# Kernel optimization log

Hardware: AMD Instinct MI355X
Metric: run time of the kernel (lower is better)

## Reference

```python
import jax, jax.numpy as jnp
import numpy as np

B, S, D, H = 4, 2048, 1024, 16
DK = D // H


def setup_inputs() -> dict:
    key = jax.random.key(0)
    ks = jax.random.split(key, 11)
    s = 1.0 / np.sqrt(D)
    return {
        "Q": jax.random.normal(ks[0], (B, S, D), jnp.float32),
        "K": jax.random.normal(ks[1], (B, S, D), jnp.float32),
        "V": jax.random.normal(ks[2], (B, S, D), jnp.float32),
        "Wq": jax.random.normal(ks[3], (D, D), jnp.float32) * s,
        "bq": jnp.zeros((D,), jnp.float32),
        "Wk": jax.random.normal(ks[4], (D, D), jnp.float32) * s,
        "bk": jnp.zeros((D,), jnp.float32),
        "Wv": jax.random.normal(ks[5], (D, D), jnp.float32) * s,
        "bv": jnp.zeros((D,), jnp.float32),
        "Wo": jax.random.normal(ks[6], (D, D), jnp.float32) * s,
        "bo": jnp.zeros((D,), jnp.float32),
    }


def reference(Q, K, V, Wq, bq, Wk, bk, Wv, bv, Wo, bo):
    # projections: [B,S,D] -> [B,H,S,DK]
    def split_heads(x):
        return x.reshape(B, -1, H, DK).transpose(0, 2, 1, 3)

    q = split_heads(Q @ Wq.T + bq)
    k = split_heads(K @ Wk.T + bk)
    v = split_heads(V @ Wv.T + bv)
    scale = 1.0 / jnp.sqrt(jnp.float32(DK))
    scores = jnp.einsum("bhqd,bhkd->bhqk", q, k) * scale
    attn = jax.nn.softmax(scores, axis=-1)  # dropout = identity (eval)
    out = jnp.einsum("bhqk,bhkd->bhqd", attn, v)
    out = out.transpose(0, 2, 1, 3).reshape(B, -1, D)
    return out @ Wo.T + bo
```

## Files before the change

### kernel.cpp

```cpp
#include <hip/hip_runtime.h>

#define SEQ    2048
#define DMODEL 1024
#define NH     16
#define DKH    64
#define MROWS  8192

typedef unsigned short u16;
typedef __bf16    bf16x8 __attribute__((ext_vector_type(8)));
typedef _Float16  f16x4  __attribute__((ext_vector_type(4)));
typedef _Float16  f16x8  __attribute__((ext_vector_type(8)));
typedef __fp16    hf16x2 __attribute__((ext_vector_type(2)));
typedef float     f32x4  __attribute__((ext_vector_type(4)));
typedef u16       u16x4  __attribute__((ext_vector_type(4)));
typedef u16       u16x8  __attribute__((ext_vector_type(8)));

__device__ __forceinline__ u16 f2b(float f) {
  union { float f; unsigned u; } v; v.f = f;
  unsigned r = v.u + 0x7fffu + ((v.u >> 16) & 1u);
  return (u16)(r >> 16);
}
__device__ __forceinline__ unsigned pk_f16(float a, float b) {
  union { hf16x2 h; unsigned u; } v;
  v.h = __builtin_amdgcn_cvt_pkrtz(a, b);
  return v.u;
}

__global__ __launch_bounds__(256) void cvt3_kernel(
    const float* __restrict__ a0, const float* __restrict__ a1, const float* __restrict__ a2,
    u16* o0, u16* o1, u16* o2, int n4) {
  int i = blockIdx.x * 256 + threadIdx.x;
  if (i >= n4) return;
  const float* in; u16* out;
  switch (blockIdx.y) {
    case 0: in = a0; out = o0; break;
    case 1: in = a1; out = o1; break;
    default: in = a2; out = o2; break;
  }
  f32x4 v = ((const f32x4*)in)[i];
  u16x4 o;
  o.x = f2b(v.x); o.y = f2b(v.y); o.z = f2b(v.z); o.w = f2b(v.w);
  ((u16x4*)out)[i] = o;
}
__global__ __launch_bounds__(256) void cvt4_kernel(
    const float* __restrict__ a0, const float* __restrict__ a1,
    const float* __restrict__ a2, const float* __restrict__ a3,
    u16* o0, u16* o1, u16* o2, u16* o3, int n4) {
  int i = blockIdx.x * 256 + threadIdx.x;
  if (i >= n4) return;
  const float* in; u16* out;
  switch (blockIdx.y) {
    case 0: in = a0; out = o0; break;
    case 1: in = a1; out = o1; break;
    case 2: in = a2; out = o2; break;
    default: in = a3; out = o3; break;
  }
  f32x4 v = ((const f32x4*)in)[i];
  u16x4 o;
  o.x = f2b(v.x); o.y = f2b(v.y); o.z = f2b(v.z); o.w = f2b(v.w);
  ((u16x4*)out)[i] = o;
}

__device__ __forceinline__ void gemm_body(
    const u16* __restrict__ A, const u16* __restrict__ W,
    const float* __restrict__ bias, void* __restrict__ outp, int mode, float oscale,
    int bx, int by, u16* smem) {
  u16* As = smem;
  u16* Bs = smem + 8192;

  const int tid  = threadIdx.x;
  const int w    = tid >> 6;
  const int lane = tid & 63;
  const int l15  = lane & 15;
  const int quad = lane >> 4;
  const int x7   = l15 & 7;
  const int n0 = bx * 128;
  const int m0 = by * 128;
  const int wm = (w >> 1) * 64;
  const int wn = (w & 1) * 64;

  f32x4 acc[4][4];
#pragma unroll
  for (int mt = 0; mt < 4; ++mt)
#pragma unroll
    for (int nt = 0; nt < 4; ++nt)
      acc[mt][nt] = (f32x4){0.f, 0.f, 0.f, 0.f};

  const int srow = w * 32 + (lane >> 3);
  const int scol = (((lane & 7) ^ (lane >> 3)) * 8);
  const size_t arow = (size_t)(m0 + srow) * DMODEL;
  const size_t brow = (size_t)(n0 + srow) * DMODEL;

  for (int ks = 0; ks < DMODEL / 64; ++ks) {
    const int k0 = ks * 64;
#pragma unroll
    for (int i = 0; i < 4; ++i) {
      __builtin_amdgcn_global_load_lds(
          (const __attribute__((address_space(1))) void*)(A + arow + (size_t)i * 8 * DMODEL + k0 + scol),
          (__attribute__((address_space(3))) void*)(&As[(w * 4 + i) * 512]),
          16, 0, 0);
      __builtin_amdgcn_global_load_lds(
          (const __attribute__((address_space(1))) void*)(W + brow + (size_t)i * 8 * DMODEL + k0 + scol),
          (__attribute__((address_space(3))) void*)(&Bs[(w * 4 + i) * 512]),
          16, 0, 0);
    }
    __syncthreads();
#pragma unroll
    for (int kk = 0; kk < 64; kk += 32) {
      const int kc = kk >> 3;
      bf16x8 af[4], bfr[4];
#pragma unroll
      for (int mt = 0; mt < 4; ++mt) {
        const int row = wm + mt * 16 + l15;
        af[mt] = *(const bf16x8*)&As[row * 64 + (((kc + quad) ^ (row & 7)) * 8)];
      }
#pragma unroll
      for (int nt = 0; nt < 4; ++nt) {
        const int row = wn + nt * 16 + l15;
        bfr[nt] = *(const bf16x8*)&Bs[row * 64 + (((kc + quad) ^ (row & 7)) * 8)];
      }
#pragma unroll
      for (int mt = 0; mt < 4; ++mt)
#pragma unroll
        for (int nt = 0; nt < 4; ++nt)
          acc[mt][nt] = __builtin_amdgcn_mfma_f32_16x16x32_bf16(af[mt], bfr[nt], acc[mt][nt], 0, 0, 0);
    }
    __syncthreads();
  }

  if (mode == 3) {
    float* o = (float*)outp;
#pragma unroll
    for (int nt = 0; nt < 4; ++nt) {
      const int col = n0 + wn + nt * 16 + l15;
      const float bv = bias[col];
#pragma unroll
      for (int mt = 0; mt < 4; ++mt) {
        const int mbase = m0 + wm + mt * 16 + quad * 4;
        f32x4 c = acc[mt][nt];
#pragma unroll
        for (int r = 0; r < 4; ++r)
          o[(size_t)(mbase + r) * DMODEL + col] = (c[r] + bv) * oscale;
      }
    }
    return;
  }

  u16* Cs = smem;
  if (mode == 0) {
#pragma unroll
    for (int nt = 0; nt < 4; ++nt) {
      const int col = n0 + wn + nt * 16 + l15;
      const float bv = bias[col];
      const int nl = wn + nt * 16 + l15;
      const int n8 = nl >> 3;
#pragma unroll
      for (int mt = 0; mt < 4; ++mt) {
        const int mb = wm + mt * 16 + quad * 4;
        f32x4 c = acc[mt][nt];
#pragma unroll
        for (int r = 0; r < 4; ++r) {
          const int m = mb + r;
          Cs[m * 128 + ((n8 ^ (m & 7)) * 8) + x7] = f2b((c[r] + bv) * oscale);
        }
      }
    }
  } else {
#pragma unroll
    for (int nt = 0; nt < 4; ++nt) {
      const int col = n0 + wn + nt * 16 + l15;
      const float bv = bias[col];
      const int nl = wn + nt * 16 + l15;
#pragma unroll
      for (int mt = 0; mt < 4; ++mt) {
        const int mb = wm + mt * 16 + quad * 4;
        f32x4 c = acc[mt][nt];
        union { u16x4 u4; unsigned u2[2]; } pk;
        pk.u2[0] = pk_f16((c[0] + bv) * oscale, (c[1] + bv) * oscale);
        pk.u2[1] = pk_f16((c[2] + bv) * oscale, (c[3] + bv) * oscale);
        *(u16x4*)&Cs[nl * 128 + (((mb >> 3) ^ (nl & 7)) * 8) + (mb & 7)] = pk.u4;
      }
    }
  }
  __syncthreads();

  const int rl   = tid >> 1;
  const int half = tid & 1;
  const int b    = m0 >> 11;
  if (mode == 0) {
    u16* o = (u16*)outp;
    const int s = (m0 + rl) & 2047;
    const int h = (n0 >> 6) + half;
    u16* orow = o + (((size_t)(b * NH + h) * SEQ + s)) * DKH;
#pragma unroll
    for (int j = 0; j < 8; ++j) {
      u16x8 v = *(const u16x8*)&Cs[rl * 128 + (((half * 8 + j) ^ (rl & 7)) * 8)];
      *(u16x8*)&orow[j * 8] = v;
    }
  } else {
    u16* o = (u16*)outp;
    const int plane = b * 1024 + n0 + rl;
    const int scol2 = (m0 & 2047) + half * 64;
    u16* orow = o + (size_t)plane * SEQ + scol2;
#pragma unroll
    for (int j = 0; j < 8; ++j) {
      u16x8 v = *(const u16x8*)&Cs[rl * 128 + (((half * 8 + j) ^ (rl & 7)) * 8)];
      *(u16x8*)&orow[j * 8] = v;
    }
  }
}

__device__ __forceinline__ void xcd_remap(int& bx, int& by) {
  const int lin = (int)blockIdx.x + (int)blockIdx.y * 8;
  const int xcd = lin & 7;
  const int idx = lin >> 3;
  by = xcd * 8 + (idx >> 3);
  bx = idx & 7;
}

__global__ __launch_bounds__(256) void gemm_kernel(
    const u16* __restrict__ A, const u16* __restrict__ W,
    const float* __restrict__ bias, void* __restrict__ outp, int mode, float oscale) {
  __shared__ __align__(16) u16 smem[16384];
  int bx, by; xcd_remap(bx, by);
  gemm_body(A, W, bias, outp, mode, oscale, bx, by, smem);
}

__global__ __launch_bounds__(256) void qkv_gemm_kernel(
    const u16* Aq, const u16* Ak, const u16* Av,
    const u16* Wq, const u16* Wk, const u16* Wv,
    const float* bq, const float* bk, const float* bv,
    u16* oq, u16* ok, u16* ov, float qscale) {
  __shared__ __align__(16) u16 smem[16384];
  const u16* A; const u16* W; const float* bias; u16* o; int mode; float sc;
  switch (blockIdx.z) {
    case 0:  A = Aq; W = Wq; bias = bq; o = oq; mode = 0; sc = qscale; break;
    case 1:  A = Ak; W = Wk; bias = bk; o = ok; mode = 0; sc = 1.f;    break;
    default: A = Av; W = Wv; bias = bv; o = ov; mode = 2; sc = 1.f;    break;
  }
  int bx, by; xcd_remap(bx, by);
  gemm_body(A, W, bias, o, mode, sc, bx, by, smem);
}

__global__ __launch_bounds__(128, 2) void attn_kernel(
    const u16* __restrict__ qh, const u16* __restrict__ kh,
    const u16* __restrict__ vt, u16* __restrict__ ao) {
  __shared__ __align__(16) u16 smem[8192];
  u16* Ks = smem;
  u16* Vs = smem + 4096;

  const int tid  = threadIdx.x;
  const int w    = tid >> 6;
  const int lane = tid & 63;
  const int l15  = lane & 15;
  const int quad = lane >> 4;
  const int x7   = l15 & 7;
  const int bh = blockIdx.y;
  const int q0 = blockIdx.x * 128;

  const u16* kbase = kh + (size_t)bh * SEQ * DKH;
  const u16* vbase = vt + (size_t)bh * DKH * SEQ;

  const int lr  = lane >> 3;
  const int lc8 = ((lane & 7) ^ lr) * 8;

  const int rbase = l15 * 64;
  const int c0 = (quad ^ x7) * 8;
  const int c1 = c0 ^ 32;

  bf16x8 qf[4][2];
#pragma unroll
  for (int g = 0; g < 4; ++g) {
    const u16* qrow = qh + ((size_t)bh * SEQ + q0 + w * 64 + g * 16 + l15) * DKH;
    qf[g][0] = *(const bf16x8*)(qrow + quad * 8);
    qf[g][1] = *(const bf16x8*)(qrow + 32 + quad * 8);
  }

  f32x4 o[4][4];
#pragma unroll
  for (int g = 0; g < 4; ++g)
#pragma unroll
    for (int dt = 0; dt < 4; ++dt) o[g][dt] = (f32x4){0.f, 0.f, 0.f, 0.f};
  float lsum[4] = {0.f, 0.f, 0.f, 0.f};

  for (int kt = 0; kt < SEQ / 64; ++kt) {
    const int k0 = kt * 64;
#pragma unroll
    for (int i = 0; i < 4; ++i) {
      const int rowb = i * 16 + w * 8;
      const int krow = rowb + lr;
      const int kkey = ((krow >> 4) & 1) * 32 + ((krow >> 2) & 3) * 8 +
                       (krow >> 5) * 4 + (krow & 3);
      __builtin_amdgcn_global_load_lds(
          (const __attribute__((address_space(1))) void*)(kbase + (size_t)(k0 + kkey) * DKH + lc8),
          (__attribute__((address_space(3))) void*)(&Ks[rowb * 64]), 16, 0, 0);
      __builtin_amdgcn_global_load_lds(
          (const __attribute__((address_space(1))) void*)(vbase + (size_t)(rowb + lr) * SEQ + k0 + lc8),
          (__attribute__((address_space(3))) void*)(&Vs[rowb * 64]), 16, 0, 0);
    }
    __syncthreads();

    bf16x8 kf[4][2];
#pragma unroll
    for (int nt = 0; nt < 4; ++nt) {
      kf[nt][0] = *(const bf16x8*)&Ks[nt * 1024 + rbase + c0];
      kf[nt][1] = *(const bf16x8*)&Ks[nt * 1024 + rbase + c1];
    }

    f16x8 pb[4][2];
#pragma unroll
    for (int g = 0; g < 4; ++g) {
      f32x4 sf[4];
      __builtin_amdgcn_s_setprio(1);
#pragma unroll
      for (int nt = 0; nt < 4; ++nt) {
        f32x4 a = (f32x4){-8.f, -8.f, -8.f, -8.f};
        a = __builtin_amdgcn_mfma_f32_16x16x32_bf16(kf[nt][0], qf[g][0], a, 0, 0, 0);
        a = __builtin_amdgcn_mfma_f32_16x16x32_bf16(kf[nt][1], qf[g][1], a, 0, 0, 0);
        sf[nt] = a;
      }
      __builtin_amdgcn_s_setprio(0);
      unsigned d0[4], d1[4];
#pragma unroll
      for (int nt = 0; nt < 4; ++nt) {
        float p0 = __builtin_amdgcn_exp2f(sf[nt][0]);
        float p1 = __builtin_amdgcn_exp2f(sf[nt][1]);
        float p2 = __builtin_amdgcn_exp2f(sf[nt][2]);
        float p3 = __builtin_amdgcn_exp2f(sf[nt][3]);
        lsum[g] += (p0 + p1) + (p2 + p3);
        d0[nt] = pk_f16(p0, p1);
        d1[nt] = pk_f16(p2, p3);
      }
#pragma unroll
      for (int b2 = 0; b2 < 2; ++b2) {
        union { f16x8 h; unsigned u[4]; } u;
        u.u[0] = d0[b2]; u.u[1] = d1[b2]; u.u[2] = d0[b2 + 2]; u.u[3] = d1[b2 + 2];
        pb[g][b2] = u.h;
      }
    }

    __builtin_amdgcn_s_setprio(1);
#pragma unroll
    for (int dt = 0; dt < 4; ++dt) {
#pragma unroll
      for (int b2 = 0; b2 < 2; ++b2) {
        const int vaddr = (dt * 16 + l15) * 64 + (((b2 * 4 + quad) ^ x7) * 8);
        f16x8 vf = *(const f16x8*)&Vs[vaddr];
#pragma unroll
        for (int g = 0; g < 4; ++g)
          o[g][dt] = __builtin_amdgcn_mfma_f32_16x16x32_f16(vf, pb[g][b2], o[g][dt], 0, 0, 0);
      }
    }
    __builtin_amdgcn_s_setprio(0);
    __syncthreads();
  }

  float inv[4];
#pragma unroll
  for (int g = 0; g < 4; ++g) {
    float l = lsum[g];
    l += __shfl_xor(l, 16);
    l += __shfl_xor(l, 32);
    inv[g] = 1.0f / l;
  }

#pragma unroll
  for (int g = 0; g < 4; ++g) {
    const int q = w * 64 + g * 16 + l15;
#pragma unroll
    for (int dt = 0; dt < 4; ++dt) {
      const int dk = dt * 16 + quad * 4;
      u16x4 pk;
      pk.x = f2b(o[g][dt][0] * inv[g]);
      pk.y = f2b(o[g][dt][1] * inv[g]);
      pk.z = f2b(o[g][dt][2] * inv[g]);
      pk.w = f2b(o[g][dt][3] * inv[g]);
      *(u16x4*)&smem[q * 64 + (((dk >> 3) ^ (q & 7)) * 8) + (dk & 7)] = pk;
    }
  }
  __syncthreads();

  const int b = bh >> 4;
  const int h = bh & 15;
  const int rr = tid >> 3;
  const int cc = tid & 7;
#pragma unroll
  for (int j = 0; j < 8; ++j) {
    const int row = j * 16 + rr;
    u16x8 v = *(const u16x8*)&smem[row * 64 + ((cc ^ (row & 7)) * 8)];
    u16* orow = ao + ((size_t)(b * SEQ + q0 + row)) * DMODEL + h * DKH + cc * 8;
    *(u16x8*)orow = v;
  }
}

extern "C" void kernel_launch(void* const* d_in, const int* in_sizes, int n_in,
                              void* d_out, int out_size, void* d_ws, size_t ws_size,
                              hipStream_t stream) {
  const float* Q  = (const float*)d_in[0];
  const float* K  = (const float*)d_in[1];
  const float* V  = (const float*)d_in[2];
  const float* Wq = (const float*)d_in[3];
  const float* bq = (const float*)d_in[4];
  const float* Wk = (const float*)d_in[5];
  const float* bk = (const float*)d_in[6];
  const float* Wv = (const float*)d_in[7];
  const float* bv = (const float*)d_in[8];
  const float* Wo = (const float*)d_in[9];
  const float* bo = (const float*)d_in[10];

  const float QSCALE = 0.18033688011112042f;
  char* ws = (char*)d_ws;
  const size_t MB = 1ull << 20;
  const int nA4 = (MROWS * DMODEL) / 4;
  const int nW4 = (DMODEL * DMODEL) / 4;
  dim3 gg(DMODEL / 128, MROWS / 128);
  dim3 ag(SEQ / 128, 4 * NH);

  if (ws_size >= 104 * MB) {
    u16* Xq  = (u16*)(ws);
    u16* Xk  = (u16*)(ws + 16 * MB);
    u16* Xv  = (u16*)(ws + 32 * MB);
    u16* Wqb = (u16*)(ws + 48 * MB);
    u16* Wkb = (u16*)(ws + 50 * MB);
    u16* Wvb = (u16*)(ws + 52 * MB);
    u16* Wob = (u16*)(ws + 54 * MB);
    u16* qh  = (u16*)(ws + 56 * MB);
    u16* kh  = (u16*)(ws + 72 * MB);
    u16* vth = (u16*)(ws + 88 * MB);
    u16* AO  = Xq;

    cvt4_kernel<<<dim3(nW4 / 256, 4), 256, 0, stream>>>(Wq, Wk, Wv, Wo, Wqb, Wkb, Wvb, Wob, nW4);
    cvt3_kernel<<<dim3(nA4 / 256, 3), 256, 0, stream>>>(Q, K, V, Xq, Xk, Xv, nA4);
    qkv_gemm_kernel<<<dim3(8, 64, 3), 256, 0, stream>>>(
        Xq, Xk, Xv, Wqb, Wkb, Wvb, bq, bk, bv, qh, kh, vth, QSCALE);
    attn_kernel<<<ag, 128, 0, stream>>>(qh, kh, vth, AO);
    gemm_kernel<<<gg, 256, 0, stream>>>(AO, Wob, bo, d_out, 3, 1.0f);
  } else {
    u16* X   = (u16*)(ws);
    u16* Wqb = (u16*)(ws + 16 * MB);
    u16* Wkb = (u16*)(ws + 18 * MB);
    u16* Wvb = (u16*)(ws + 20 * MB);
    u16* Wob = (u16*)(ws + 22 * MB);
    u16* qh  = (u16*)(ws + 24 * MB);
    u16* kh  = (u16*)(ws + 40 * MB);
    u16* vth = (u16*)(ws + 56 * MB);

    cvt4_kernel<<<dim3(nW4 / 256, 4), 256, 0, stream>>>(Wq, Wk, Wv, Wo, Wqb, Wkb, Wvb, Wob, nW4);
    cvt3_kernel<<<dim3(nA4 / 256, 1), 256, 0, stream>>>(Q, Q, Q, X, X, X, nA4);
    gemm_kernel<<<gg, 256, 0, stream>>>(X, Wqb, bq, qh, 0, QSCALE);
    cvt3_kernel<<<dim3(nA4 / 256, 1), 256, 0, stream>>>(K, K, K, X, X, X, nA4);
    gemm_kernel<<<gg, 256, 0, stream>>>(X, Wkb, bk, kh, 0, 1.0f);
    cvt3_kernel<<<dim3(nA4 / 256, 1), 256, 0, stream>>>(V, V, V, X, X, X, nA4);
    gemm_kernel<<<gg, 256, 0, stream>>>(X, Wvb, bv, vth, 2, 1.0f);
    attn_kernel<<<ag, 128, 0, stream>>>(qh, kh, vth, X);
    gemm_kernel<<<gg, 256, 0, stream>>>(X, Wob, bo, d_out, 3, 1.0f);
  }
}
```

Measured before the change: 342.6 us.

## Split attention KV range across wave pairs with LDS reduction and remap blocks

Doubles the attention block to 256 threads (4 waves). Two waves handle the 128 query rows over the first half of the key sequence and two handle the second half, so each block runs 16 KV iterations instead of 32. The partial O accumulators and row sums are merged through LDS. Block indices are also remapped so that neighbouring blocks spread across (b,h) heads, which targets XCD/L2 locality. The aim is more waves in flight per block, at the cost of extra LDS, an extra reduction step with syncs, and possible lower occupancy from the larger shared memory footprint.

```diff
diff --git a/kernel.cpp b/kernel.cpp
--- a/kernel.cpp
+++ b/kernel.cpp
@@ -242,12 +242,10 @@
   gemm_body(A, W, bias, o, mode, sc, bx, by, smem);
 }
 
-__global__ __launch_bounds__(128, 2) void attn_kernel(
+__global__ __launch_bounds__(256, 4) void attn_kernel(
     const u16* __restrict__ qh, const u16* __restrict__ kh,
     const u16* __restrict__ vt, u16* __restrict__ ao) {
-  __shared__ __align__(16) u16 smem[8192];
-  u16* Ks = smem;
-  u16* Vs = smem + 4096;
+  __shared__ __align__(16) u16 smem[16896];
 
   const int tid  = threadIdx.x;
   const int w    = tid >> 6;
@@ -255,8 +253,10 @@
   const int l15  = lane & 15;
   const int quad = lane >> 4;
   const int x7   = l15 & 7;
-  const int bh = blockIdx.y;
-  const int q0 = blockIdx.x * 128;
+
+  const int lin = (int)blockIdx.x + ((int)blockIdx.y << 4);
+  const int bh  = (lin & 7) * 8 + ((lin >> 3) >> 4);
+  const int q0  = ((lin >> 3) & 15) * 128;
 
   const u16* kbase = kh + (size_t)bh * SEQ * DKH;
   const u16* vbase = vt + (size_t)bh * DKH * SEQ;
@@ -268,10 +268,13 @@
   const int c0 = (quad ^ x7) * 8;
   const int c1 = c0 ^ 32;
 
+  const int qhalf = w & 1;
+  const int khalf = w >> 1;
+
   bf16x8 qf[4][2];
 #pragma unroll
   for (int g = 0; g < 4; ++g) {
-    const u16* qrow = qh + ((size_t)bh * SEQ + q0 + w * 64 + g * 16 + l15) * DKH;
+    const u16* qrow = qh + ((size_t)bh * SEQ + q0 + qhalf * 64 + g * 16 + l15) * DKH;
     qf[g][0] = *(const bf16x8*)(qrow + quad * 8);
     qf[g][1] = *(const bf16x8*)(qrow + 32 + quad * 8);
   }
@@ -283,22 +286,36 @@
     for (int dt = 0; dt < 4; ++dt) o[g][dt] = (f32x4){0.f, 0.f, 0.f, 0.f};
   float lsum[4] = {0.f, 0.f, 0.f, 0.f};
 
-  for (int kt = 0; kt < SEQ / 64; ++kt) {
-    const int k0 = kt * 64;
-#pragma unroll
-    for (int i = 0; i < 4; ++i) {
-      const int rowb = i * 16 + w * 8;
-      const int krow = rowb + lr;
-      const int kkey = ((krow >> 4) & 1) * 32 + ((krow >> 2) & 3) * 8 +
-                       (krow >> 5) * 4 + (krow & 3);
-      __builtin_amdgcn_global_load_lds(
-          (const __attribute__((address_space(1))) void*)(kbase + (size_t)(k0 + kkey) * DKH + lc8),
-          (__attribute__((address_space(3))) void*)(&Ks[rowb * 64]), 16, 0, 0);
-      __builtin_amdgcn_global_load_lds(
-          (const __attribute__((address_space(1))) void*)(vbase + (size_t)(rowb + lr) * SEQ + k0 + lc8),
-          (__attribute__((address_space(3))) void*)(&Vs[rowb * 64]), 16, 0, 0);
+  const int sth = w & 1;
+  const int stv = w >> 1;
+  u16* dstb = smem + sth * 8192 + stv * 4096;
+
+  for (int kt = 0; kt < SEQ / 128; ++kt) {
+    const int sk0 = sth * 1024 + kt * 64;
+    if (stv == 0) {
+#pragma unroll
+      for (int i = 0; i < 8; ++i) {
+        const int rowb = i * 8;
+        const int krow = rowb + lr;
+        const int kkey = ((krow >> 4) & 1) * 32 + ((krow >> 2) & 3) * 8 +
+                         (krow >> 5) * 4 + (krow & 3);
+        __builtin_amdgcn_global_load_lds(
+            (const __attribute__((address_space(1))) void*)(kbase + (size_t)(sk0 + kkey) * DKH + lc8),
+            (__attribute__((address_space(3))) void*)(&dstb[rowb * 64]), 16, 0, 0);
+      }
+    } else {
+#pragma unroll
+      for (int i = 0; i < 8; ++i) {
+        const int rowb = i * 8;
+        __builtin_amdgcn_global_load_lds(
+            (const __attribute__((address_space(1))) void*)(vbase + (size_t)(rowb + lr) * SEQ + sk0 + lc8),
+            (__attribute__((address_space(3))) void*)(&dstb[rowb * 64]), 16, 0, 0);
+      }
     }
     __syncthreads();
+
+    const u16* Ks = smem + khalf * 8192;
+    const u16* Vs = Ks + 4096;
 
     bf16x8 kf[4][2];
 #pragma unroll
@@ -355,38 +372,76 @@
     __syncthreads();
   }
 
-  float inv[4];
+  float lh[4];
 #pragma unroll
   for (int g = 0; g < 4; ++g) {
     float l = lsum[g];
     l += __shfl_xor(l, 16);
     l += __shfl_xor(l, 32);
-    inv[g] = 1.0f / l;
-  }
-
-#pragma unroll
-  for (int g = 0; g < 4; ++g) {
-    const int q = w * 64 + g * 16 + l15;
-#pragma unroll
-    for (int dt = 0; dt < 4; ++dt) {
-      const int dk = dt * 16 + quad * 4;
-      u16x4 pk;
-      pk.x = f2b(o[g][dt][0] * inv[g]);
-      pk.y = f2b(o[g][dt][1] * inv[g]);
-      pk.z = f2b(o[g][dt][2] * inv[g]);
-      pk.w = f2b(o[g][dt][3] * inv[g]);
-      *(u16x4*)&smem[q * 64 + (((dk >> 3) ^ (q & 7)) * 8) + (dk & 7)] = pk;
+    lh[g] = l;
+  }
+
+  float* ldsO = (float*)smem;
+  float* ldsL = (float*)&smem[16384];
+  const int p = qhalf;
+  if (w >= 2) {
+#pragma unroll
+    for (int g = 0; g < 4; ++g) {
+#pragma unroll
+      for (int dt = 0; dt < 4; ++dt) {
+        const int q  = g * 16 + l15;
+        const int dk = dt * 16 + quad * 4;
+        *(f32x4*)&ldsO[p * 4096 + q * 64 + (dk ^ ((q & 7) << 3))] = o[g][dt];
+      }
+    }
+    if (quad == 0) {
+#pragma unroll
+      for (int g = 0; g < 4; ++g) ldsL[p * 64 + g * 16 + l15] = lh[g];
     }
   }
   __syncthreads();
 
-  const int b = bh >> 4;
-  const int h = bh & 15;
+  float inv[4];
+  if (w < 2) {
+#pragma unroll
+    for (int g = 0; g < 4; ++g) {
+#pragma unroll
+      for (int dt = 0; dt < 4; ++dt) {
+        const int q  = g * 16 + l15;
+        const int dk = dt * 16 + quad * 4;
+        f32x4 t = *(const f32x4*)&ldsO[p * 4096 + q * 64 + (dk ^ ((q & 7) << 3))];
+        o[g][dt] += t;
+      }
+      inv[g] = 1.0f / (lh[g] + ldsL[p * 64 + g * 16 + l15]);
+    }
+  }
+  __syncthreads();
+
+  if (w < 2) {
+#pragma unroll
+    for (int g = 0; g < 4; ++g) {
+      const int q = qhalf * 64 + g * 16 + l15;
+#pragma unroll
+      for (int dt = 0; dt < 4; ++dt) {
+        const int dk = dt * 16 + quad * 4;
+        u16x4 pk;
+        pk.x = f2b(o[g][dt][0] * inv[g]);
+        pk.y = f2b(o[g][dt][1] * inv[g]);
+        pk.z = f2b(o[g][dt][2] * inv[g]);
+        pk.w = f2b(o[g][dt][3] * inv[g]);
+        *(u16x4*)&smem[q * 64 + (((dk >> 3) ^ (q & 7)) * 8) + (dk & 7)] = pk;
+      }
+    }
+  }
+  __syncthreads();
+
+  const int b  = bh >> 4;
+  const int h  = bh & 15;
   const int rr = tid >> 3;
   const int cc = tid & 7;
 #pragma unroll
-  for (int j = 0; j < 8; ++j) {
-    const int row = j * 16 + rr;
+  for (int j = 0; j < 4; ++j) {
+    const int row = j * 32 + rr;
     u16x8 v = *(const u16x8*)&smem[row * 64 + ((cc ^ (row & 7)) * 8)];
     u16* orow = ao + ((size_t)(b * SEQ + q0 + row)) * DMODEL + h * DKH + cc * 8;
     *(u16x8*)orow = v;
@@ -433,7 +488,7 @@
     cvt3_kernel<<<dim3(nA4 / 256, 3), 256, 0, stream>>>(Q, K, V, Xq, Xk, Xv, nA4);
     qkv_gemm_kernel<<<dim3(8, 64, 3), 256, 0, stream>>>(
         Xq, Xk, Xv, Wqb, Wkb, Wvb, bq, bk, bv, qh, kh, vth, QSCALE);
-    attn_kernel<<<ag, 128, 0, stream>>>(qh, kh, vth, AO);
+    attn_kernel<<<ag, 256, 0, stream>>>(qh, kh, vth, AO);
     gemm_kernel<<<gg, 256, 0, stream>>>(AO, Wob, bo, d_out, 3, 1.0f);
   } else {
     u16* X   = (u16*)(ws);
@@ -452,7 +507,7 @@
     gemm_kernel<<<gg, 256, 0, stream>>>(X, Wkb, bk, kh, 0, 1.0f);
     cvt3_kernel<<<dim3(nA4 / 256, 1), 256, 0, stream>>>(V, V, V, X, X, X, nA4);
     gemm_kernel<<<gg, 256, 0, stream>>>(X, Wvb, bv, vth, 2, 1.0f);
-    attn_kernel<<<ag, 128, 0, stream>>>(qh, kh, vth, X);
+    attn_kernel<<<ag, 256, 0, stream>>>(qh, kh, vth, X);
     gemm_kernel<<<gg, 256, 0, stream>>>(X, Wob, bo, d_out, 3, 1.0f);
   }
 }
```

Measured after the change: 650.9 us. +90.0%, slower.

## Double-buffer K/V tiles in attention kernel with async global-to-LDS prefetch

Applied to the files above, without the earlier changes.

The attention kernel gets a second LDS buffer. It issues the global_load_lds copies for the next K/V tile before computing the current one, and uses vmcnt waits plus raw barriers instead of __syncthreads. This is meant to hide global memory latency behind the MFMA work. LDS use per block doubles to 32KB, which may limit occupancy. Correctness also relies on the manual vmcnt(8) counting matching the eight loads each stage issues.

```diff
diff --git a/kernel.cpp b/kernel.cpp
--- a/kernel.cpp
+++ b/kernel.cpp
@@ -245,9 +245,7 @@
 __global__ __launch_bounds__(128, 2) void attn_kernel(
     const u16* __restrict__ qh, const u16* __restrict__ kh,
     const u16* __restrict__ vt, u16* __restrict__ ao) {
-  __shared__ __align__(16) u16 smem[8192];
-  u16* Ks = smem;
-  u16* Vs = smem + 4096;
+  __shared__ __align__(16) u16 smem[16384];
 
   const int tid  = threadIdx.x;
   const int w    = tid >> 6;
@@ -275,16 +273,16 @@
     qf[g][0] = *(const bf16x8*)(qrow + quad * 8);
     qf[g][1] = *(const bf16x8*)(qrow + 32 + quad * 8);
   }
-
-  f32x4 o[4][4];
-#pragma unroll
-  for (int g = 0; g < 4; ++g)
-#pragma unroll
-    for (int dt = 0; dt < 4; ++dt) o[g][dt] = (f32x4){0.f, 0.f, 0.f, 0.f};
-  float lsum[4] = {0.f, 0.f, 0.f, 0.f};
-
-  for (int kt = 0; kt < SEQ / 64; ++kt) {
-    const int k0 = kt * 64;
+#pragma unroll
+  for (int g = 0; g < 4; ++g) {
+    asm volatile("" : "+v"(qf[g][0]));
+    asm volatile("" : "+v"(qf[g][1]));
+  }
+  asm volatile("s_waitcnt vmcnt(0)" ::: "memory");
+
+  auto stage = [&](int buf, int k0) {
+    u16* Ksb = smem + buf * 8192;
+    u16* Vsb = Ksb + 4096;
 #pragma unroll
     for (int i = 0; i < 4; ++i) {
       const int rowb = i * 16 + w * 8;
@@ -293,12 +291,34 @@
                        (krow >> 5) * 4 + (krow & 3);
       __builtin_amdgcn_global_load_lds(
           (const __attribute__((address_space(1))) void*)(kbase + (size_t)(k0 + kkey) * DKH + lc8),
-          (__attribute__((address_space(3))) void*)(&Ks[rowb * 64]), 16, 0, 0);
+          (__attribute__((address_space(3))) void*)(&Ksb[rowb * 64]), 16, 0, 0);
       __builtin_amdgcn_global_load_lds(
           (const __attribute__((address_space(1))) void*)(vbase + (size_t)(rowb + lr) * SEQ + k0 + lc8),
-          (__attribute__((address_space(3))) void*)(&Vs[rowb * 64]), 16, 0, 0);
-    }
-    __syncthreads();
+          (__attribute__((address_space(3))) void*)(&Vsb[rowb * 64]), 16, 0, 0);
+    }
+  };
+
+  f32x4 o[4][4];
+#pragma unroll
+  for (int g = 0; g < 4; ++g)
+#pragma unroll
+    for (int dt = 0; dt < 4; ++dt) o[g][dt] = (f32x4){0.f, 0.f, 0.f, 0.f};
+  float lsum[4] = {0.f, 0.f, 0.f, 0.f};
+
+  stage(0, 0);
+  int cur = 0;
+
+  for (int kt = 0; kt < SEQ / 64; ++kt) {
+    if (kt + 1 < SEQ / 64) {
+      stage(cur ^ 1, (kt + 1) * 64);
+      asm volatile("s_waitcnt vmcnt(8)" ::: "memory");
+    } else {
+      asm volatile("s_waitcnt vmcnt(0)" ::: "memory");
+    }
+    __builtin_amdgcn_s_barrier();
+
+    const u16* Ks = smem + cur * 8192;
+    const u16* Vs = Ks + 4096;
 
     bf16x8 kf[4][2];
 #pragma unroll
@@ -352,7 +372,10 @@
       }
     }
     __builtin_amdgcn_s_setprio(0);
-    __syncthreads();
+
+    asm volatile("" ::: "memory");
+    __builtin_amdgcn_s_barrier();
+    cur ^= 1;
   }
 
   float inv[4];
@@ -364,6 +387,7 @@
     inv[g] = 1.0f / l;
   }
 
+  __syncthreads();
 #pragma unroll
   for (int g = 0; g < 4; ++g) {
     const int q = w * 64 + g * 16 + l15;
```

After: 338.9 us. No clear change (-1.1%).
